# Kernel optimization log

Hardware: AMD Instinct MI355X
Metric: run time of the kernel (lower is better)

## Reference

```python
import jax, jax.numpy as jnp
import numpy as np

N_NODES = 131072
N_EDGES = 1048576
D_IN, D_HID, D_OUT = 64, 64, 3
NUM_GRAPHS = 32


def setup_inputs() -> dict:
    key = jax.random.key(0)
    k = jax.random.split(key, 6)
    x = jax.random.normal(k[0], (N_NODES, D_IN), dtype=jnp.float32)
    edge_index = jax.random.randint(k[1], (2, N_EDGES), 0, N_NODES, dtype=jnp.int64)
    # batch assignment: 32 graphs of 4096 contiguous nodes each
    batch = jnp.repeat(jnp.arange(NUM_GRAPHS, dtype=jnp.int32), N_NODES // NUM_GRAPHS)
    W1 = jax.random.normal(k[2], (D_IN, D_HID), dtype=jnp.float32) * (1.0 / np.sqrt(D_IN))
    b1 = jnp.zeros((D_HID,), dtype=jnp.float32)
    W2 = jax.random.normal(k[3], (D_HID, D_OUT), dtype=jnp.float32) * (1.0 / np.sqrt(D_HID))
    b2 = jnp.zeros((D_OUT,), dtype=jnp.float32)
    return {"x": x, "edge_index": edge_index, "batch": batch,
            "W1": W1, "b1": b1, "W2": W2, "b2": b2}


def _gcn_conv(x, W, b, row, col, deg_inv_sqrt):
    # PyG GCNConv: x' = D^{-1/2}(A+I)D^{-1/2} X W + b (self-loops added)
    h = x @ W  # [N, d_out]
    norm = deg_inv_sqrt[row] * deg_inv_sqrt[col]  # [E]
    msg = h[row] * norm[:, None]                  # gather + scale
    agg = jax.ops.segment_sum(msg, col, num_segments=x.shape[0])
    # self-loop contribution: norm_ii = deg_inv_sqrt[i]^2
    agg = agg + h * (deg_inv_sqrt * deg_inv_sqrt)[:, None]
    return agg + b


def reference(x, edge_index, batch, W1, b1, W2, b2):
    N = x.shape[0]
    row, col = edge_index[0], edge_index[1]
    # degree at target nodes, including self-loops (+1)
    ones = jnp.ones((row.shape[0],), dtype=x.dtype)
    deg = jax.ops.segment_sum(ones, col, num_segments=N) + 1.0
    deg_inv_sqrt = jax.lax.rsqrt(deg)

    h = _gcn_conv(x, W1, b1, row, col, deg_inv_sqrt)
    h = jax.nn.relu(h)
    # F.dropout in eval mode is identity
    h = _gcn_conv(h, W2, b2, row, col, deg_inv_sqrt)

    # global_mean_pool over batch vector
    batch = batch.astype(jnp.int32)
    sums = jax.ops.segment_sum(h, batch, num_segments=NUM_GRAPHS)
    counts = jax.ops.segment_sum(jnp.ones((N,), dtype=h.dtype), batch, num_segments=NUM_GRAPHS)
    return sums / jnp.maximum(counts, 1.0)[:, None]
```

## Files before the change

### kernel.cpp

```cpp
#include <hip/hip_runtime.h>

#define NN 131072
#define NE 1048576
#define DD 64
#define NG 32
#define NPG 4096
#define NB 512
#define CAPB 2560

__device__ __forceinline__ float blo(unsigned int u) { return __uint_as_float(u << 16); }
__device__ __forceinline__ float bhi(unsigned int u) { return __uint_as_float(u & 0xFFFF0000u); }
__device__ __forceinline__ unsigned short f2bf(float f) {
  unsigned int u = __float_as_uint(f);
  return (unsigned short)((u + 0x7FFFu + ((u >> 16) & 1u)) >> 16);
}
__device__ __forceinline__ unsigned int pack2(float a, float b) {
  return (unsigned int)f2bf(a) | ((unsigned int)f2bf(b) << 16);
}

extern "C" __global__ __launch_bounds__(256) void k_gemm1(
    const float* __restrict__ x, const float* __restrict__ W1, unsigned short* __restrict__ h1b,
    int* __restrict__ bcursor, const float* __restrict__ b2, float* __restrict__ out) {
  __shared__ float4 wl[DD * 16];
  int t = threadIdx.x;
  if (blockIdx.x < 2) {
    int i = blockIdx.x * 256 + t;
    bcursor[i] = i * CAPB;
    if (i < NG * 3) out[i] = b2[i % 3];
  }
  for (int i = t; i < DD * 16; i += 256) wl[i] = reinterpret_cast<const float4*>(W1)[i];
  __syncthreads();
  int jc = t & 3;
  int rg = t >> 2;
  size_t rbase = (size_t)blockIdx.x * 128 + (size_t)rg * 2;
  const float4* xp = reinterpret_cast<const float4*>(x + rbase * DD);
  float4 acc[2][4];
#pragma unroll
  for (int r = 0; r < 2; ++r)
#pragma unroll
    for (int j = 0; j < 4; ++j) acc[r][j] = make_float4(0.f, 0.f, 0.f, 0.f);
#pragma unroll 2
  for (int kk = 0; kk < 16; ++kk) {
    float4 a0 = xp[kk];
    float4 a1 = xp[16 + kk];
#pragma unroll
    for (int j = 0; j < 4; ++j) {
      float4 w0 = wl[(4 * kk + 0) * 16 + jc * 4 + j];
      float4 w1 = wl[(4 * kk + 1) * 16 + jc * 4 + j];
      float4 w2 = wl[(4 * kk + 2) * 16 + jc * 4 + j];
      float4 w3 = wl[(4 * kk + 3) * 16 + jc * 4 + j];
      acc[0][j].x += a0.x * w0.x + a0.y * w1.x + a0.z * w2.x + a0.w * w3.x;
      acc[0][j].y += a0.x * w0.y + a0.y * w1.y + a0.z * w2.y + a0.w * w3.y;
      acc[0][j].z += a0.x * w0.z + a0.y * w1.z + a0.z * w2.z + a0.w * w3.z;
      acc[0][j].w += a0.x * w0.w + a0.y * w1.w + a0.z * w2.w + a0.w * w3.w;
      acc[1][j].x += a1.x * w0.x + a1.y * w1.x + a1.z * w2.x + a1.w * w3.x;
      acc[1][j].y += a1.x * w0.y + a1.y * w1.y + a1.z * w2.y + a1.w * w3.y;
      acc[1][j].z += a1.x * w0.z + a1.y * w1.z + a1.z * w2.z + a1.w * w3.z;
      acc[1][j].w += a1.x * w0.w + a1.y * w1.w + a1.z * w2.w + a1.w * w3.w;
    }
  }
#pragma unroll
  for (int r = 0; r < 2; ++r) {
    uint4* hp = reinterpret_cast<uint4*>(h1b + (rbase + r) * DD + jc * 16);
    hp[0] = make_uint4(pack2(acc[r][0].x, acc[r][0].y), pack2(acc[r][0].z, acc[r][0].w),
                       pack2(acc[r][1].x, acc[r][1].y), pack2(acc[r][1].z, acc[r][1].w));
    hp[1] = make_uint4(pack2(acc[r][2].x, acc[r][2].y), pack2(acc[r][2].z, acc[r][2].w),
                       pack2(acc[r][3].x, acc[r][3].y), pack2(acc[r][3].z, acc[r][3].w));
  }
}

extern "C" __global__ __launch_bounds__(256) void k_bscatter(
    const int* __restrict__ row, const int* __restrict__ col, int* __restrict__ bcursor,
    int* __restrict__ ebuf) {
  __shared__ int sh[NB];
  __shared__ int sb[NB];
  int t = threadIdx.x;
  sh[t] = 0; sh[t + 256] = 0;
  __syncthreads();
  int cols[8], lr[8];
#pragma unroll
  for (int k = 0; k < 8; ++k) {
    int e = blockIdx.x * 2048 + k * 256 + t;
    cols[k] = col[e];
    lr[k] = atomicAdd(&sh[cols[k] >> 8], 1);
  }
  __syncthreads();
  int h0 = sh[t];
  sb[t] = h0 ? atomicAdd(&bcursor[t], h0) : 0;
  int h1 = sh[t + 256];
  sb[t + 256] = h1 ? atomicAdd(&bcursor[t + 256], h1) : 0;
  __syncthreads();
#pragma unroll
  for (int k = 0; k < 8; ++k) {
    int e = blockIdx.x * 2048 + k * 256 + t;
    int key = cols[k] >> 8;
    int pos = sb[key] + lr[k];
    if (pos < (key + 1) * CAPB)
      ebuf[pos] = (row[e] << 8) | (cols[k] & 255);
  }
}

extern "C" __global__ __launch_bounds__(256) void k_blocal(
    const int* __restrict__ ebuf, const int* __restrict__ bcursor, int* __restrict__ cnt,
    float* __restrict__ dis, int* __restrict__ starts, int* __restrict__ nbr) {
  __shared__ int sh[256];
  __shared__ int sx[256];
  int b = blockIdx.x, t = threadIdx.x;
  int bs = b * CAPB;
  int n_e = bcursor[b] - bs;
  if (n_e > CAPB) n_e = CAPB;
  sh[t] = 0;
  __syncthreads();
  for (int i = t; i < n_e; i += 256) atomicAdd(&sh[ebuf[bs + i] & 255], 1);
  __syncthreads();
  int v = sh[t];
  sx[t] = v;
  __syncthreads();
  for (int off = 1; off < 256; off <<= 1) {
    int u = (t >= off) ? sx[t - off] : 0;
    __syncthreads();
    sx[t] += u;
    __syncthreads();
  }
  int st = bs + sx[t] - v;
  int node = b * 256 + t;
  cnt[node] = v;
  dis[node] = rsqrtf((float)v + 1.0f);
  starts[node] = st;
  sx[t] = st;
  __syncthreads();
  for (int i = t; i < n_e; i += 256) {
    int ed = ebuf[bs + i];
    int pos = atomicAdd(&sx[ed & 255], 1);
    nbr[pos] = ed >> 8;
  }
}

extern "C" __global__ __launch_bounds__(256) void k_agg1f(
    const unsigned short* __restrict__ h1b, const int* __restrict__ starts,
    const int* __restrict__ cnt, const int* __restrict__ nbr, const float* __restrict__ dis,
    const float* __restrict__ b1, const float* __restrict__ W2, float4* __restrict__ h2) {
  __shared__ int2 sed[4][2][32];
  int lane = threadIdx.x & 63;
  int wid = threadIdx.x >> 6;
  int h = lane >> 5;
  int hl = lane & 31;
  int node = blockIdx.x * 8 + wid * 2 + h;
  int start = starts[node];
  int deg = cnt[node];
  float dc = dis[node];
  int nb = node;
  float w = 0.f;
  if (hl < deg) {
    nb = nbr[start + hl];
    w = dis[nb] * dc;
  } else if (hl == deg) {
    w = 1.0f / (float)(deg + 1);
  }
  sed[wid][h][hl] = make_int2(nb, __float_as_int(w));
  int m = (deg < 32) ? (deg + 1) : 32;
  int mw = max(m, __shfl_xor(m, 32));
  int mw4 = (mw + 3) & ~3;
  asm volatile("s_waitcnt lgkmcnt(0)" ::: "memory");
  __builtin_amdgcn_sched_barrier(0);
  const unsigned int* h1d = reinterpret_cast<const unsigned int*>(h1b);
  const int2* sp = sed[wid][h];
  float a0 = 0.f, a1 = 0.f;
  for (int e = 0; e < mw4; e += 4) {
    int2 e0 = sp[e + 0];
    int2 e1 = sp[e + 1];
    int2 e2 = sp[e + 2];
    int2 e3 = sp[e + 3];
    unsigned int u0 = h1d[(size_t)e0.x * 32 + hl];
    unsigned int u1 = h1d[(size_t)e1.x * 32 + hl];
    unsigned int u2 = h1d[(size_t)e2.x * 32 + hl];
    unsigned int u3 = h1d[(size_t)e3.x * 32 + hl];
    float q0 = __int_as_float(e0.y), q1 = __int_as_float(e1.y);
    float q2 = __int_as_float(e2.y), q3 = __int_as_float(e3.y);
    a0 += q0 * blo(u0) + q1 * blo(u1) + q2 * blo(u2) + q3 * blo(u3);
    a1 += q0 * bhi(u0) + q1 * bhi(u1) + q2 * bhi(u2) + q3 * bhi(u3);
  }
  if (deg >= 32) {
    for (int eo = 32; eo < deg; ++eo) {
      int r = nbr[start + eo];
      float q = dis[r] * dc;
      unsigned int u = h1d[(size_t)r * 32 + hl];
      a0 += q * blo(u);
      a1 += q * bhi(u);
    }
    float q = 1.0f / (float)(deg + 1);
    unsigned int u = h1d[(size_t)node * 32 + hl];
    a0 += q * blo(u);
    a1 += q * bhi(u);
  }
  float z0 = fmaxf(a0 + b1[2 * hl + 0], 0.f);
  float z1 = fmaxf(a1 + b1[2 * hl + 1], 0.f);
  float v0 = z0 * W2[(2 * hl) * 3 + 0] + z1 * W2[(2 * hl + 1) * 3 + 0];
  float v1 = z0 * W2[(2 * hl) * 3 + 1] + z1 * W2[(2 * hl + 1) * 3 + 1];
  float v2 = z0 * W2[(2 * hl) * 3 + 2] + z1 * W2[(2 * hl + 1) * 3 + 2];
#pragma unroll
  for (int off = 16; off > 0; off >>= 1) {
    v0 += __shfl_xor(v0, off);
    v1 += __shfl_xor(v1, off);
    v2 += __shfl_xor(v2, off);
  }
  if (hl == 0) h2[node] = make_float4(v0, v1, v2, 0.f);
}

extern "C" __global__ __launch_bounds__(256) void k_agg2pool(
    const float4* __restrict__ h2, const int* __restrict__ starts, const int* __restrict__ cnt,
    const int* __restrict__ nbr, const float* __restrict__ dis, float* __restrict__ out) {
  int n = blockIdx.x * 256 + threadIdx.x;
  int start = starts[n], deg = cnt[n], end = start + deg;
  float dc = dis[n];
  float selfw = 1.0f / (float)(deg + 1);
  float4 hs = h2[n];
  float s0 = hs.x * selfw, s1 = hs.y * selfw, s2 = hs.z * selfw;
  int e = start;
  for (; e + 2 <= end; e += 2) {
    int n0 = nbr[e], n1 = nbr[e + 1];
    float4 h0 = h2[n0], h1 = h2[n1];
    float w0 = dis[n0] * dc, w1 = dis[n1] * dc;
    s0 += w0 * h0.x + w1 * h1.x;
    s1 += w0 * h0.y + w1 * h1.y;
    s2 += w0 * h0.z + w1 * h1.z;
  }
  if (e < end) {
    int n0 = nbr[e];
    float4 h0 = h2[n0];
    float w0 = dis[n0] * dc;
    s0 += w0 * h0.x;
    s1 += w0 * h0.y;
    s2 += w0 * h0.z;
  }
  __shared__ float red[3][256];
  int t = threadIdx.x;
  red[0][t] = s0; red[1][t] = s1; red[2][t] = s2;
  __syncthreads();
  for (int off = 128; off > 0; off >>= 1) {
    if (t < off) {
      red[0][t] += red[0][t + off];
      red[1][t] += red[1][t + off];
      red[2][t] += red[2][t + off];
    }
    __syncthreads();
  }
  if (t == 0) {
    int g = blockIdx.x >> 4;
    const float inv = 1.0f / (float)NPG;
    atomicAdd(&out[g * 3 + 0], red[0][0] * inv);
    atomicAdd(&out[g * 3 + 1], red[1][0] * inv);
    atomicAdd(&out[g * 3 + 2], red[2][0] * inv);
  }
}

extern "C" void kernel_launch(void* const* d_in, const int* in_sizes, int n_in,
                              void* d_out, int out_size, void* d_ws, size_t ws_size,
                              hipStream_t stream) {
  const float* x  = (const float*)d_in[0];
  const int*   ei = (const int*)d_in[1];
  const float* W1 = (const float*)d_in[3];
  const float* b1 = (const float*)d_in[4];
  const float* W2 = (const float*)d_in[5];
  const float* b2 = (const float*)d_in[6];
  const int* row = ei;
  const int* col = ei + NE;
  float* out = (float*)d_out;

  char* ws = (char*)d_ws;
  int*   cnt     = (int*)(ws + 0);
  float* dis     = (float*)(ws + (1u << 19));
  int*   starts  = (int*)(ws + (2u << 19));
  int*   bcursor = (int*)(ws + (3u << 19));
  int*   ebuf    = (int*)(ws + (4u << 19));
  int*   nbr     = (int*)(ws + (1u << 23));
  unsigned short* h1b = (unsigned short*)(ws + (1u << 24));
  float4* h2     = (float4*)(ws + (1u << 25));

  k_gemm1<<<NN / 128, 256, 0, stream>>>(x, W1, h1b, bcursor, b2, out);
  k_bscatter<<<NE / 2048, 256, 0, stream>>>(row, col, bcursor, ebuf);
  k_blocal<<<NB, 256, 0, stream>>>(ebuf, bcursor, cnt, dis, starts, nbr);
  k_agg1f<<<NN / 8, 256, 0, stream>>>(h1b, starts, cnt, nbr, dis, b1, W2, h2);
  k_agg2pool<<<NN / 256, 256, 0, stream>>>(h2, starts, cnt, nbr, dis, out);
}
```

Baseline: 109.7 us.

## Pre-scale GEMM rows by inverse sqrt degree to drop per-edge weights

```diff
diff --git a/kernel.cpp b/kernel.cpp
--- a/kernel.cpp
+++ b/kernel.cpp
@@ -18,15 +18,81 @@
   return (unsigned int)f2bf(a) | ((unsigned int)f2bf(b) << 16);
 }
 
-extern "C" __global__ __launch_bounds__(256) void k_gemm1(
-    const float* __restrict__ x, const float* __restrict__ W1, unsigned short* __restrict__ h1b,
-    int* __restrict__ bcursor, const float* __restrict__ b2, float* __restrict__ out) {
+extern "C" __global__ __launch_bounds__(256) void k_bscatter(
+    const int* __restrict__ row, const int* __restrict__ col, int* __restrict__ bcursor,
+    int* __restrict__ ebuf) {
+  __shared__ int sh[NB];
+  __shared__ int sb[NB];
+  int t = threadIdx.x;
+  sh[t] = 0; sh[t + 256] = 0;
+  __syncthreads();
+  int cols[8], lr[8];
+#pragma unroll
+  for (int k = 0; k < 8; ++k) {
+    int e = blockIdx.x * 2048 + k * 256 + t;
+    cols[k] = col[e];
+    lr[k] = atomicAdd(&sh[cols[k] >> 8], 1);
+  }
+  __syncthreads();
+  int h0 = sh[t];
+  sb[t] = t * CAPB + (h0 ? atomicAdd(&bcursor[t], h0) : 0);
+  int h1 = sh[t + 256];
+  sb[t + 256] = (t + 256) * CAPB + (h1 ? atomicAdd(&bcursor[t + 256], h1) : 0);
+  __syncthreads();
+#pragma unroll
+  for (int k = 0; k < 8; ++k) {
+    int e = blockIdx.x * 2048 + k * 256 + t;
+    int key = cols[k] >> 8;
+    int pos = sb[key] + lr[k];
+    if (pos < (key + 1) * CAPB)
+      ebuf[pos] = (row[e] << 8) | (cols[k] & 255);
+  }
+}
+
+extern "C" __global__ __launch_bounds__(256) void k_blocal(
+    const int* __restrict__ ebuf, const int* __restrict__ bcursor, int* __restrict__ cnt,
+    float* __restrict__ dis, int* __restrict__ starts, int* __restrict__ nbr) {
+  __shared__ int sh[256];
+  __shared__ int sx[256];
+  int b = blockIdx.x, t = threadIdx.x;
+  int bs = b * CAPB;
+  int n_e = bcursor[b];
+  if (n_e > CAPB) n_e = CAPB;
+  sh[t] = 0;
+  __syncthreads();
+  for (int i = t; i < n_e; i += 256) atomicAdd(&sh[ebuf[bs + i] & 255], 1);
+  __syncthreads();
+  int v = sh[t];
+  sx[t] = v;
+  __syncthreads();
+  for (int off = 1; off < 256; off <<= 1) {
+    int u = (t >= off) ? sx[t - off] : 0;
+    __syncthreads();
+    sx[t] += u;
+    __syncthreads();
+  }
+  int st = bs + sx[t] - v;
+  int node = b * 256 + t;
+  cnt[node] = v;
+  dis[node] = rsqrtf((float)v + 1.0f);
+  starts[node] = st;
+  sx[t] = st;
+  __syncthreads();
+  for (int i = t; i < n_e; i += 256) {
+    int ed = ebuf[bs + i];
+    int pos = atomicAdd(&sx[ed & 255], 1);
+    nbr[pos] = ed >> 8;
+  }
+}
+
+extern "C" __global__ __launch_bounds__(256) void k_gemm1s(
+    const float* __restrict__ x, const float* __restrict__ W1, const float* __restrict__ dis,
+    unsigned short* __restrict__ h1b, const float* __restrict__ b2, float* __restrict__ out) {
   __shared__ float4 wl[DD * 16];
   int t = threadIdx.x;
-  if (blockIdx.x < 2) {
-    int i = blockIdx.x * 256 + t;
-    bcursor[i] = i * CAPB;
-    if (i < NG * 3) out[i] = b2[i % 3];
+  if (blockIdx.x == 0) {
+    if (t < 32) reinterpret_cast<unsigned int*>(h1b)[(size_t)NN * 32 + t] = 0u;
+    if (t < NG * 3) out[t] = b2[t % 3];
   }
   for (int i = t; i < DD * 16; i += 256) wl[i] = reinterpret_cast<const float4*>(W1)[i];
   __syncthreads();
@@ -34,6 +100,7 @@
   int rg = t >> 2;
   size_t rbase = (size_t)blockIdx.x * 128 + (size_t)rg * 2;
   const float4* xp = reinterpret_cast<const float4*>(x + rbase * DD);
+  float2 sc = *reinterpret_cast<const float2*>(dis + rbase);
   float4 acc[2][4];
 #pragma unroll
   for (int r = 0; r < 2; ++r)
@@ -61,78 +128,12 @@
   }
 #pragma unroll
   for (int r = 0; r < 2; ++r) {
+    float s = r ? sc.y : sc.x;
     uint4* hp = reinterpret_cast<uint4*>(h1b + (rbase + r) * DD + jc * 16);
-    hp[0] = make_uint4(pack2(acc[r][0].x, acc[r][0].y), pack2(acc[r][0].z, acc[r][0].w),
-                       pack2(acc[r][1].x, acc[r][1].y), pack2(acc[r][1].z, acc[r][1].w));
-    hp[1] = make_uint4(pack2(acc[r][2].x, acc[r][2].y), pack2(acc[r][2].z, acc[r][2].w),
-                       pack2(acc[r][3].x, acc[r][3].y), pack2(acc[r][3].z, acc[r][3].w));
-  }
-}
-
-extern "C" __global__ __launch_bounds__(256) void k_bscatter(
-    const int* __restrict__ row, const int* __restrict__ col, int* __restrict__ bcursor,
-    int* __restrict__ ebuf) {
-  __shared__ int sh[NB];
-  __shared__ int sb[NB];
-  int t = threadIdx.x;
-  sh[t] = 0; sh[t + 256] = 0;
-  __syncthreads();
-  int cols[8], lr[8];
-#pragma unroll
-  for (int k = 0; k < 8; ++k) {
-    int e = blockIdx.x * 2048 + k * 256 + t;
-    cols[k] = col[e];
-    lr[k] = atomicAdd(&sh[cols[k] >> 8], 1);
-  }
-  __syncthreads();
-  int h0 = sh[t];
-  sb[t] = h0 ? atomicAdd(&bcursor[t], h0) : 0;
-  int h1 = sh[t + 256];
-  sb[t + 256] = h1 ? atomicAdd(&bcursor[t + 256], h1) : 0;
-  __syncthreads();
-#pragma unroll
-  for (int k = 0; k < 8; ++k) {
-    int e = blockIdx.x * 2048 + k * 256 + t;
-    int key = cols[k] >> 8;
-    int pos = sb[key] + lr[k];
-    if (pos < (key + 1) * CAPB)
-      ebuf[pos] = (row[e] << 8) | (cols[k] & 255);
-  }
-}
-
-extern "C" __global__ __launch_bounds__(256) void k_blocal(
-    const int* __restrict__ ebuf, const int* __restrict__ bcursor, int* __restrict__ cnt,
-    float* __restrict__ dis, int* __restrict__ starts, int* __restrict__ nbr) {
-  __shared__ int sh[256];
-  __shared__ int sx[256];
-  int b = blockIdx.x, t = threadIdx.x;
-  int bs = b * CAPB;
-  int n_e = bcursor[b] - bs;
-  if (n_e > CAPB) n_e = CAPB;
-  sh[t] = 0;
-  __syncthreads();
-  for (int i = t; i < n_e; i += 256) atomicAdd(&sh[ebuf[bs + i] & 255], 1);
-  __syncthreads();
-  int v = sh[t];
-  sx[t] = v;
-  __syncthreads();
-  for (int off = 1; off < 256; off <<= 1) {
-    int u = (t >= off) ? sx[t - off] : 0;
-    __syncthreads();
-    sx[t] += u;
-    __syncthreads();
-  }
-  int st = bs + sx[t] - v;
-  int node = b * 256 + t;
-  cnt[node] = v;
-  dis[node] = rsqrtf((float)v + 1.0f);
-  starts[node] = st;
-  sx[t] = st;
-  __syncthreads();
-  for (int i = t; i < n_e; i += 256) {
-    int ed = ebuf[bs + i];
-    int pos = atomicAdd(&sx[ed & 255], 1);
-    nbr[pos] = ed >> 8;
+    hp[0] = make_uint4(pack2(acc[r][0].x * s, acc[r][0].y * s), pack2(acc[r][0].z * s, acc[r][0].w * s),
+                       pack2(acc[r][1].x * s, acc[r][1].y * s), pack2(acc[r][1].z * s, acc[r][1].w * s));
+    hp[1] = make_uint4(pack2(acc[r][2].x * s, acc[r][2].y * s), pack2(acc[r][2].z * s, acc[r][2].w * s),
+                       pack2(acc[r][3].x * s, acc[r][3].y * s), pack2(acc[r][3].z * s, acc[r][3].w * s));
   }
 }
 
@@ -140,7 +141,7 @@
     const unsigned short* __restrict__ h1b, const int* __restrict__ starts,
     const int* __restrict__ cnt, const int* __restrict__ nbr, const float* __restrict__ dis,
     const float* __restrict__ b1, const float* __restrict__ W2, float4* __restrict__ h2) {
-  __shared__ int2 sed[4][2][32];
+  __shared__ int sed[4][2][32];
   int lane = threadIdx.x & 63;
   int wid = threadIdx.x >> 6;
   int h = lane >> 5;
@@ -149,90 +150,79 @@
   int start = starts[node];
   int deg = cnt[node];
   float dc = dis[node];
-  int nb = node;
-  float w = 0.f;
-  if (hl < deg) {
-    nb = nbr[start + hl];
-    w = dis[nb] * dc;
-  } else if (hl == deg) {
-    w = 1.0f / (float)(deg + 1);
-  }
-  sed[wid][h][hl] = make_int2(nb, __float_as_int(w));
+  int nb = NN;
+  if (hl < deg) nb = nbr[start + hl];
+  else if (hl == deg) nb = node;
+  sed[wid][h][hl] = nb;
   int m = (deg < 32) ? (deg + 1) : 32;
   int mw = max(m, __shfl_xor(m, 32));
   int mw4 = (mw + 3) & ~3;
   asm volatile("s_waitcnt lgkmcnt(0)" ::: "memory");
   __builtin_amdgcn_sched_barrier(0);
   const unsigned int* h1d = reinterpret_cast<const unsigned int*>(h1b);
-  const int2* sp = sed[wid][h];
+  const int* sp = sed[wid][h];
   float a0 = 0.f, a1 = 0.f;
   for (int e = 0; e < mw4; e += 4) {
-    int2 e0 = sp[e + 0];
-    int2 e1 = sp[e + 1];
-    int2 e2 = sp[e + 2];
-    int2 e3 = sp[e + 3];
-    unsigned int u0 = h1d[(size_t)e0.x * 32 + hl];
-    unsigned int u1 = h1d[(size_t)e1.x * 32 + hl];
-    unsigned int u2 = h1d[(size_t)e2.x * 32 + hl];
-    unsigned int u3 = h1d[(size_t)e3.x * 32 + hl];
-    float q0 = __int_as_float(e0.y), q1 = __int_as_float(e1.y);
-    float q2 = __int_as_float(e2.y), q3 = __int_as_float(e3.y);
-    a0 += q0 * blo(u0) + q1 * blo(u1) + q2 * blo(u2) + q3 * blo(u3);
-    a1 += q0 * bhi(u0) + q1 * bhi(u1) + q2 * bhi(u2) + q3 * bhi(u3);
+    int n0 = sp[e + 0], n1 = sp[e + 1], n2 = sp[e + 2], n3 = sp[e + 3];
+    unsigned int u0 = h1d[(size_t)n0 * 32 + hl];
+    unsigned int u1 = h1d[(size_t)n1 * 32 + hl];
+    unsigned int u2 = h1d[(size_t)n2 * 32 + hl];
+    unsigned int u3 = h1d[(size_t)n3 * 32 + hl];
+    a0 += blo(u0) + blo(u1) + blo(u2) + blo(u3);
+    a1 += bhi(u0) + bhi(u1) + bhi(u2) + bhi(u3);
   }
   if (deg >= 32) {
     for (int eo = 32; eo < deg; ++eo) {
       int r = nbr[start + eo];
-      float q = dis[r] * dc;
       unsigned int u = h1d[(size_t)r * 32 + hl];
-      a0 += q * blo(u);
-      a1 += q * bhi(u);
+      a0 += blo(u);
+      a1 += bhi(u);
     }
-    float q = 1.0f / (float)(deg + 1);
     unsigned int u = h1d[(size_t)node * 32 + hl];
-    a0 += q * blo(u);
-    a1 += q * bhi(u);
-  }
-  float z0 = fmaxf(a0 + b1[2 * hl + 0], 0.f);
-  float z1 = fmaxf(a1 + b1[2 * hl + 1], 0.f);
-  float v0 = z0 * W2[(2 * hl) * 3 + 0] + z1 * W2[(2 * hl + 1) * 3 + 0];
-  float v1 = z0 * W2[(2 * hl) * 3 + 1] + z1 * W2[(2 * hl + 1) * 3 + 1];
-  float v2 = z0 * W2[(2 * hl) * 3 + 2] + z1 * W2[(2 * hl + 1) * 3 + 2];
+    a0 += blo(u);
+    a1 += bhi(u);
+  }
+  float2 bb = *reinterpret_cast<const float2*>(b1 + 2 * hl);
+  float z0 = fmaxf(fmaf(dc, a0, bb.x), 0.f);
+  float z1 = fmaxf(fmaf(dc, a1, bb.y), 0.f);
+  float2 wa = *reinterpret_cast<const float2*>(W2 + 6 * hl);
+  float2 wb = *reinterpret_cast<const float2*>(W2 + 6 * hl + 2);
+  float2 wc = *reinterpret_cast<const float2*>(W2 + 6 * hl + 4);
+  float v0 = z0 * wa.x + z1 * wb.y;
+  float v1 = z0 * wa.y + z1 * wc.x;
+  float v2 = z0 * wb.x + z1 * wc.y;
 #pragma unroll
   for (int off = 16; off > 0; off >>= 1) {
     v0 += __shfl_xor(v0, off);
     v1 += __shfl_xor(v1, off);
     v2 += __shfl_xor(v2, off);
   }
-  if (hl == 0) h2[node] = make_float4(v0, v1, v2, 0.f);
+  if (hl == 0) h2[node] = make_float4(v0 * dc, v1 * dc, v2 * dc, dc);
 }
 
 extern "C" __global__ __launch_bounds__(256) void k_agg2pool(
     const float4* __restrict__ h2, const int* __restrict__ starts, const int* __restrict__ cnt,
-    const int* __restrict__ nbr, const float* __restrict__ dis, float* __restrict__ out) {
+    const int* __restrict__ nbr, float* __restrict__ out) {
   int n = blockIdx.x * 256 + threadIdx.x;
   int start = starts[n], deg = cnt[n], end = start + deg;
-  float dc = dis[n];
-  float selfw = 1.0f / (float)(deg + 1);
   float4 hs = h2[n];
-  float s0 = hs.x * selfw, s1 = hs.y * selfw, s2 = hs.z * selfw;
+  float s0 = hs.x, s1 = hs.y, s2 = hs.z;
   int e = start;
   for (; e + 2 <= end; e += 2) {
     int n0 = nbr[e], n1 = nbr[e + 1];
     float4 h0 = h2[n0], h1 = h2[n1];
-    float w0 = dis[n0] * dc, w1 = dis[n1] * dc;
-    s0 += w0 * h0.x + w1 * h1.x;
-    s1 += w0 * h0.y + w1 * h1.y;
-    s2 += w0 * h0.z + w1 * h1.z;
+    s0 += h0.x + h1.x;
+    s1 += h0.y + h1.y;
+    s2 += h0.z + h1.z;
   }
   if (e < end) {
-    int n0 = nbr[e];
-    float4 h0 = h2[n0];
-    float w0 = dis[n0] * dc;
-    s0 += w0 * h0.x;
-    s1 += w0 * h0.y;
-    s2 += w0 * h0.z;
-  }
+    float4 h0 = h2[nbr[e]];
+    s0 += h0.x;
+    s1 += h0.y;
+    s2 += h0.z;
+  }
+  float dn = hs.w;
+  s0 *= dn; s1 *= dn; s2 *= dn;
   __shared__ float red[3][256];
   int t = threadIdx.x;
   red[0][t] = s0; red[1][t] = s1; red[2][t] = s2;
@@ -275,11 +265,12 @@
   int*   ebuf    = (int*)(ws + (4u << 19));
   int*   nbr     = (int*)(ws + (1u << 23));
   unsigned short* h1b = (unsigned short*)(ws + (1u << 24));
-  float4* h2     = (float4*)(ws + (1u << 25));
-
-  k_gemm1<<<NN / 128, 256, 0, stream>>>(x, W1, h1b, bcursor, b2, out);
+  float4* h2     = (float4*)(ws + (1u << 25) + 4096u);
+
+  hipMemsetAsync(bcursor, 0, NB * sizeof(int), stream);
   k_bscatter<<<NE / 2048, 256, 0, stream>>>(row, col, bcursor, ebuf);
   k_blocal<<<NB, 256, 0, stream>>>(ebuf, bcursor, cnt, dis, starts, nbr);
+  k_gemm1s<<<NN / 128, 256, 0, stream>>>(x, W1, dis, h1b, b2, out);
   k_agg1f<<<NN / 8, 256, 0, stream>>>(h1b, starts, cnt, nbr, dis, b1, W2, h2);
-  k_agg2pool<<<NN / 256, 256, 0, stream>>>(h2, starts, cnt, nbr, dis, out);
-}
+  k_agg2pool<<<NN / 256, 256, 0, stream>>>(h2, starts, cnt, nbr, out);
+}
```

After: 108.4 us. Within noise of the previous version (-1.2%).
